# Optimization experiments

Measured on AMD Instinct MI355X. Metric: run time of the kernel, lower is better.

Reference implementation:

```python
import jax, jax.numpy as jnp
import numpy as np

C_CLIP = 10.0  # Bello et al. logit clipping constant (init arg C)


def setup_inputs() -> dict:
    key = jax.random.key(0)
    k1, k2, k3, k4, k5 = jax.random.split(key, 5)
    B, S, D = 64, 2048, 512
    scale = 1.0 / np.sqrt(D)  # ~torch Linear default init scale
    src = jax.random.normal(k1, (B, S, D), dtype=jnp.float32)
    tgt = jax.random.normal(k2, (B, 1, D), dtype=jnp.float32)
    W_q = jax.random.normal(k3, (D, D), dtype=jnp.float32) * scale
    W_ref = jax.random.normal(k4, (D, D), dtype=jnp.float32) * scale
    v = jax.random.uniform(k5, (D,), dtype=jnp.float32)  # uniform_(0, 1) as in source
    return {"src": src, "tgt": tgt, "W_q": W_q, "W_ref": W_ref, "v": v}


def reference(src, tgt, W_q, W_ref, v):
    # h = tanh(W_q(tgt) + W_ref(src))  -> [B, S, D] (tgt broadcasts over S)
    h = jnp.tanh(tgt @ W_q.T + src @ W_ref.T)
    # u = bmm(v, h^T) -> [B, 1, S]
    u = jnp.einsum("bsd,d->bs", h, v)[:, None, :]
    # logit clipping: C * tanh(u)
    logit = C_CLIP * jnp.tanh(u)
    probs = jax.nn.softmax(logit, axis=-1)  # [B, 1, S]
    # d_prime = bmm(probs, src) -> [B, 1, D]  ('Sup' path glimpse)
    d_prime = jnp.einsum("bqs,bsd->bqd", probs, src)
    return (d_prime, probs, logit)
```

## Files before the change

kernel.cpp:

```cpp
#include <hip/hip_runtime.h>
#include <math.h>

#define NB 64
#define NS 2048
#define ND 512
#define MTOT (NB * NS)
#define CCLIP 10.0f

typedef _Float16 f16x8 __attribute__((ext_vector_type(8)));
typedef _Float16 f16x4 __attribute__((ext_vector_type(4)));
typedef float f32x4 __attribute__((ext_vector_type(4)));

__device__ __forceinline__ void gl2lds16(const void* g, void* l) {
  __builtin_amdgcn_global_load_lds(
      (const __attribute__((address_space(1))) void*)(uintptr_t)g,
      (__attribute__((address_space(3))) void*)(uintptr_t)l, 16, 0, 0);
}

__device__ __forceinline__ float tanh_fast(float x) {
  float e = __expf(2.f * x);
  return 1.f - 2.f * __builtin_amdgcn_rcpf(e + 1.f);
}

__global__ __launch_bounds__(256) void cvtw_kernel(
    const float4* __restrict__ w4, _Float16* __restrict__ WhA) {
  const int idx = blockIdx.x * 256 + threadIdx.x;
  const int d = idx >> 7;
  const int k = (idx & 127) << 2;
  float4 x = w4[idx];
  f16x4 o;
  o[0] = (_Float16)x.x; o[1] = (_Float16)x.y;
  o[2] = (_Float16)x.z; o[3] = (_Float16)x.w;
  const int kt = k >> 5;
  const int kg = (k >> 3) & 3;
  const int h = k & 7;
  *(f16x4*)(WhA + ((size_t)((kt * 4 + kg) * 512 + d) * 8 + h)) = o;
}

__global__ __launch_bounds__(256) void qk_kernel(const float* __restrict__ tgt,
                                                 const float* __restrict__ Wq,
                                                 float* __restrict__ q_ws) {
  const int b = blockIdx.x >> 1;
  const int d = ((blockIdx.x & 1) << 8) + threadIdx.x;
  __shared__ float tl[ND];
  tl[threadIdx.x] = tgt[b * ND + threadIdx.x];
  tl[threadIdx.x + 256] = tgt[b * ND + threadIdx.x + 256];
  __syncthreads();
  const float4* wr = (const float4*)(Wq + (size_t)d * ND);
  float acc = 0.f;
#pragma unroll 8
  for (int k4 = 0; k4 < ND / 4; ++k4) {
    float4 w4 = wr[k4];
    acc += w4.x * tl[4 * k4 + 0] + w4.y * tl[4 * k4 + 1] +
           w4.z * tl[4 * k4 + 2] + w4.w * tl[4 * k4 + 3];
  }
  q_ws[b * ND + d] = acc;
}

__global__ __launch_bounds__(256, 2) void gemm_kernel(
    const float* __restrict__ src, const _Float16* __restrict__ WhA,
    const float* __restrict__ q_ws, const float* __restrict__ v,
    float* __restrict__ out_logit, float* __restrict__ out_probs_w) {
  __shared__ __align__(16) _Float16 sA[4 * 64 * 8];
  __shared__ __align__(16) _Float16 sB[4 * 512 * 8];
  __shared__ float ured[4 * 64];

  const int tid = threadIdx.x;
  const int lane = tid & 63;
  const int w = tid >> 6;
  const int s0 = blockIdx.x << 6;
  const int bb = blockIdx.x >> 5;

  const int quad = lane >> 4;
  const int l15 = lane & 15;

  const int ar = tid & 63;
  const int akg = tid >> 6;
  const float4* ap =
      (const float4*)(src + ((size_t)(s0 + ar) << 9)) + akg * 2;
  _Float16* aw = sA + (akg * 64 + ar) * 8;

  const char* gB = (const char*)WhA;

  f32x4 acc[4][8];
#pragma unroll
  for (int i = 0; i < 4; ++i)
#pragma unroll
    for (int j = 0; j < 8; ++j) acc[i][j] = (f32x4){0.f, 0.f, 0.f, 0.f};

  for (int kt = 0; kt < 16; ++kt) {
    __syncthreads();
#pragma unroll
    for (int i = 0; i < 8; ++i) {
      const int c = w * 8 + i;
      gl2lds16(gB + (size_t)kt * 32768 + c * 1024 + lane * 16,
               (char*)sB + c * 1024);
    }
    float4 x0 = ap[kt * 8];
    float4 x1 = ap[kt * 8 + 1];
    f16x8 h;
    h[0] = (_Float16)x0.x; h[1] = (_Float16)x0.y;
    h[2] = (_Float16)x0.z; h[3] = (_Float16)x0.w;
    h[4] = (_Float16)x1.x; h[5] = (_Float16)x1.y;
    h[6] = (_Float16)x1.z; h[7] = (_Float16)x1.w;
    *(f16x8*)aw = h;
    __syncthreads();

    f16x8 af[4], bf[8];
#pragma unroll
    for (int i = 0; i < 4; ++i)
      af[i] = *(const f16x8*)(sA + (quad * 64 + 16 * i + l15) * 8);
#pragma unroll
    for (int j = 0; j < 8; ++j)
      bf[j] = *(const f16x8*)(sB + (quad * 512 + w * 128 + 16 * j + l15) * 8);
#pragma unroll
    for (int i = 0; i < 4; ++i)
#pragma unroll
      for (int j = 0; j < 8; ++j)
        acc[i][j] = __builtin_amdgcn_mfma_f32_16x16x32_f16(af[i], bf[j],
                                                           acc[i][j], 0, 0, 0);
  }

  float pu[4][4];
#pragma unroll
  for (int i = 0; i < 4; ++i)
#pragma unroll
    for (int r = 0; r < 4; ++r) pu[i][r] = 0.f;

#pragma unroll
  for (int j = 0; j < 8; ++j) {
    const int dl = w * 128 + 16 * j + l15;
    const float qq = q_ws[bb * ND + dl];
    const float vv = v[dl];
#pragma unroll
    for (int i = 0; i < 4; ++i) {
      f32x4 a = acc[i][j];
#pragma unroll
      for (int r = 0; r < 4; ++r) pu[i][r] += tanh_fast(a[r] + qq) * vv;
    }
  }

#pragma unroll
  for (int i = 0; i < 4; ++i)
#pragma unroll
    for (int r = 0; r < 4; ++r) {
      float x = pu[i][r];
      x += __shfl_xor(x, 1, 16);
      x += __shfl_xor(x, 2, 16);
      x += __shfl_xor(x, 4, 16);
      x += __shfl_xor(x, 8, 16);
      pu[i][r] = x;
    }

  if (l15 == 0) {
#pragma unroll
    for (int i = 0; i < 4; ++i)
#pragma unroll
      for (int r = 0; r < 4; ++r)
        ured[w * 64 + 16 * i + quad * 4 + r] = pu[i][r];
  }
  __syncthreads();
  if (tid < 64) {
    const float u =
        ured[tid] + ured[64 + tid] + ured[128 + tid] + ured[192 + tid];
    const float lg = CCLIP * tanhf(u);
    out_logit[s0 + tid] = lg;
    out_probs_w[s0 + tid] = expf(lg - CCLIP);
  }
}

__global__ __launch_bounds__(256) void dp_kernel(const float* __restrict__ src,
                                                 const float* __restrict__ w_ws,
                                                 float* __restrict__ dp_ws) {
  const int blk = blockIdx.x;
  const int b = blk >> 4;
  const int ch = (blk >> 1) & 7;
  const int half = blk & 1;
  const int tid = threadIdx.x;
  const int row0 = b * NS + ch * 256;
  const float* base = src + ((size_t)row0 << 9) + (half << 8) + tid;
  float a = 0.f;
#pragma unroll 8
  for (int s = 0; s < 256; ++s) a += w_ws[row0 + s] * base[(size_t)s << 9];
  dp_ws[(size_t)blk * 256 + tid] = a;
}

__global__ __launch_bounds__(256) void fin_kernel(
    const float* __restrict__ dp_ws, float* __restrict__ out_dp,
    float* __restrict__ out_probs) {
  const int b = blockIdx.x;
  const int tid = threadIdx.x;
  __shared__ float red[4];
  __shared__ float s_inv;

  float x = 0.f;
  for (int idx = tid; idx < NS; idx += 256) x += out_probs[b * NS + idx];
#pragma unroll
  for (int m = 32; m; m >>= 1) x += __shfl_xor(x, m, 64);
  if ((tid & 63) == 0) red[tid >> 6] = x;
  __syncthreads();
  if (tid == 0) s_inv = 1.f / (red[0] + red[1] + red[2] + red[3]);
  __syncthreads();
  const float inv = s_inv;

  for (int idx = tid; idx < NS; idx += 256)
    out_probs[b * NS + idx] *= inv;

  for (int d = tid; d < ND; d += 256) {
    const int half = d >> 8;
    const int dl = d & 255;
    float acc = 0.f;
#pragma unroll
    for (int ch = 0; ch < 8; ++ch)
      acc += dp_ws[(size_t)(((b * 8 + ch) << 1) + half) * 256 + dl];
    out_dp[b * ND + d] = acc * inv;
  }
}

extern "C" void kernel_launch(void* const* d_in, const int* in_sizes, int n_in,
                              void* d_out, int out_size, void* d_ws,
                              size_t ws_size, hipStream_t stream) {
  const float* src = (const float*)d_in[0];
  const float* tgt = (const float*)d_in[1];
  const float* Wq = (const float*)d_in[2];
  const float* Wref = (const float*)d_in[3];
  const float* v = (const float*)d_in[4];

  float* out = (float*)d_out;
  float* out_dp = out;
  float* out_probs = out + NB * ND;
  float* out_logit = out + NB * ND + NB * NS;

  char* ws = (char*)d_ws;
  _Float16* WhA = (_Float16*)ws;
  float* q_ws = (float*)(ws + 524288);
  float* dp_ws = (float*)(ws + 655360);

  cvtw_kernel<<<256, 256, 0, stream>>>((const float4*)Wref, WhA);
  qk_kernel<<<2 * NB, 256, 0, stream>>>(tgt, Wq, q_ws);
  gemm_kernel<<<MTOT / 64, 256, 0, stream>>>(src, WhA, q_ws, v, out_logit,
                                             out_probs);
  dp_kernel<<<NB * 16, 256, 0, stream>>>(src, out_probs, dp_ws);
  fin_kernel<<<NB, 256, 0, stream>>>(dp_ws, out_dp, out_probs);
}
```

Baseline: 482.0 us.

## Fuse weighted src reduction into GEMM and double-buffer LDS tiles

The separate dp_kernel is removed. Each GEMM block now computes its own exp-weighted sum of its 64 src rows right after the logits, while those rows are likely still in cache, and writes per-block partials that fin_kernel reduces over 32 chunks. The GEMM main loop double-buffers the A and B LDS tiles, prefetching the next k-tile while MFMAs run, so there is one barrier per iteration instead of two. The A-load thread mapping is also changed so each row is read contiguously. The cost is double the LDS footprint, which may reduce occupancy, and a larger dp workspace.

```diff
diff --git a/kernel.cpp b/kernel.cpp
--- a/kernel.cpp
+++ b/kernel.cpp
@@ -60,10 +60,12 @@
 __global__ __launch_bounds__(256, 2) void gemm_kernel(
     const float* __restrict__ src, const _Float16* __restrict__ WhA,
     const float* __restrict__ q_ws, const float* __restrict__ v,
-    float* __restrict__ out_logit, float* __restrict__ out_probs_w) {
-  __shared__ __align__(16) _Float16 sA[4 * 64 * 8];
-  __shared__ __align__(16) _Float16 sB[4 * 512 * 8];
+    float* __restrict__ out_logit, float* __restrict__ out_probs_w,
+    float* __restrict__ dp_ws) {
+  __shared__ __align__(16) _Float16 sA[2][4 * 64 * 8];
+  __shared__ __align__(16) _Float16 sB[2][4 * 512 * 8];
   __shared__ float ured[4 * 64];
+  __shared__ float wsh[64];
 
   const int tid = threadIdx.x;
   const int lane = tid & 63;
@@ -74,11 +76,11 @@
   const int quad = lane >> 4;
   const int l15 = lane & 15;
 
-  const int ar = tid & 63;
-  const int akg = tid >> 6;
+  const int ar = tid >> 2;
+  const int akg = tid & 3;
   const float4* ap =
       (const float4*)(src + ((size_t)(s0 + ar) << 9)) + akg * 2;
-  _Float16* aw = sA + (akg * 64 + ar) * 8;
+  const int aoff = (akg * 64 + ar) * 8;
 
   const char* gB = (const char*)WhA;
 
@@ -88,37 +90,61 @@
 #pragma unroll
     for (int j = 0; j < 8; ++j) acc[i][j] = (f32x4){0.f, 0.f, 0.f, 0.f};
 
-  for (int kt = 0; kt < 16; ++kt) {
-    __syncthreads();
-#pragma unroll
-    for (int i = 0; i < 8; ++i) {
-      const int c = w * 8 + i;
-      gl2lds16(gB + (size_t)kt * 32768 + c * 1024 + lane * 16,
-               (char*)sB + c * 1024);
-    }
-    float4 x0 = ap[kt * 8];
-    float4 x1 = ap[kt * 8 + 1];
+#pragma unroll
+  for (int i = 0; i < 8; ++i) {
+    const int c = w * 8 + i;
+    gl2lds16(gB + c * 1024 + lane * 16, (char*)&sB[0][0] + c * 1024);
+  }
+  {
+    float4 x0 = ap[0];
+    float4 x1 = ap[1];
     f16x8 h;
     h[0] = (_Float16)x0.x; h[1] = (_Float16)x0.y;
     h[2] = (_Float16)x0.z; h[3] = (_Float16)x0.w;
     h[4] = (_Float16)x1.x; h[5] = (_Float16)x1.y;
     h[6] = (_Float16)x1.z; h[7] = (_Float16)x1.w;
-    *(f16x8*)aw = h;
-    __syncthreads();
-
+    *(f16x8*)(&sA[0][0] + aoff) = h;
+  }
+  __syncthreads();
+
+  int buf = 0;
+  for (int kt = 0; kt < 16; ++kt) {
+    const int nb = buf ^ 1;
+    float4 x0, x1;
+    if (kt < 15) {
+#pragma unroll
+      for (int i = 0; i < 8; ++i) {
+        const int c = w * 8 + i;
+        gl2lds16(gB + (size_t)(kt + 1) * 32768 + c * 1024 + lane * 16,
+                 (char*)&sB[nb][0] + c * 1024);
+      }
+      x0 = ap[(kt + 1) * 8];
+      x1 = ap[(kt + 1) * 8 + 1];
+    }
     f16x8 af[4], bf[8];
 #pragma unroll
     for (int i = 0; i < 4; ++i)
-      af[i] = *(const f16x8*)(sA + (quad * 64 + 16 * i + l15) * 8);
+      af[i] = *(const f16x8*)(&sA[buf][0] + (quad * 64 + 16 * i + l15) * 8);
 #pragma unroll
     for (int j = 0; j < 8; ++j)
-      bf[j] = *(const f16x8*)(sB + (quad * 512 + w * 128 + 16 * j + l15) * 8);
+      bf[j] = *(const f16x8*)(&sB[buf][0] +
+                              (quad * 512 + w * 128 + 16 * j + l15) * 8);
 #pragma unroll
     for (int i = 0; i < 4; ++i)
 #pragma unroll
       for (int j = 0; j < 8; ++j)
         acc[i][j] = __builtin_amdgcn_mfma_f32_16x16x32_f16(af[i], bf[j],
                                                            acc[i][j], 0, 0, 0);
+    if (kt < 15) {
+      f16x8 h;
+      h[0] = (_Float16)x0.x; h[1] = (_Float16)x0.y;
+      h[2] = (_Float16)x0.z; h[3] = (_Float16)x0.w;
+      h[4] = (_Float16)x1.x; h[5] = (_Float16)x1.y;
+      h[6] = (_Float16)x1.z; h[7] = (_Float16)x1.w;
+      *(f16x8*)(&sA[nb][0] + aoff) = h;
+    }
+    __syncthreads();
+    buf = nb;
   }
 
   float pu[4][4];
@@ -165,24 +191,34 @@
         ured[tid] + ured[64 + tid] + ured[128 + tid] + ured[192 + tid];
     const float lg = CCLIP * tanhf(u);
     out_logit[s0 + tid] = lg;
-    out_probs_w[s0 + tid] = expf(lg - CCLIP);
-  }
-}
-
-__global__ __launch_bounds__(256) void dp_kernel(const float* __restrict__ src,
-                                                 const float* __restrict__ w_ws,
-                                                 float* __restrict__ dp_ws) {
-  const int blk = blockIdx.x;
-  const int b = blk >> 4;
-  const int ch = (blk >> 1) & 7;
-  const int half = blk & 1;
-  const int tid = threadIdx.x;
-  const int row0 = b * NS + ch * 256;
-  const float* base = src + ((size_t)row0 << 9) + (half << 8) + tid;
-  float a = 0.f;
-#pragma unroll 8
-  for (int s = 0; s < 256; ++s) a += w_ws[row0 + s] * base[(size_t)s << 9];
-  dp_ws[(size_t)blk * 256 + tid] = a;
+    const float wexp = expf(lg - CCLIP);
+    out_probs_w[s0 + tid] = wexp;
+    wsh[tid] = wexp;
+  }
+  __syncthreads();
+
+  const int c4 = tid & 127;
+  const int half = tid >> 7;
+  const float4* sp = (const float4*)(src + ((size_t)s0 << 9)) + c4;
+  float dx = 0.f, dy = 0.f, dz = 0.f, dw = 0.f;
+  const int r0 = half << 5;
+#pragma unroll 4
+  for (int r = r0; r < r0 + 32; ++r) {
+    const float wr = wsh[r];
+    const float4 x = sp[(size_t)r * 128];
+    dx += wr * x.x; dy += wr * x.y; dz += wr * x.z; dw += wr * x.w;
+  }
+  float4* red4 = (float4*)&sA[0][0];
+  if (half) {
+    float4 o; o.x = dx; o.y = dy; o.z = dz; o.w = dw;
+    red4[c4] = o;
+  }
+  __syncthreads();
+  if (!half) {
+    float4 o = red4[c4];
+    o.x += dx; o.y += dy; o.z += dz; o.w += dw;
+    *(float4*)(dp_ws + (size_t)blockIdx.x * ND + (c4 << 2)) = o;
+  }
 }
 
 __global__ __launch_bounds__(256) void fin_kernel(
@@ -207,12 +243,10 @@
     out_probs[b * NS + idx] *= inv;
 
   for (int d = tid; d < ND; d += 256) {
-    const int half = d >> 8;
-    const int dl = d & 255;
     float acc = 0.f;
-#pragma unroll
-    for (int ch = 0; ch < 8; ++ch)
-      acc += dp_ws[(size_t)(((b * 8 + ch) << 1) + half) * 256 + dl];
+#pragma unroll 8
+    for (int ch = 0; ch < 32; ++ch)
+      acc += dp_ws[(size_t)(b * 32 + ch) * ND + d];
     out_dp[b * ND + d] = acc * inv;
   }
 }
@@ -239,7 +273,6 @@
   cvtw_kernel<<<256, 256, 0, stream>>>((const float4*)Wref, WhA);
   qk_kernel<<<2 * NB, 256, 0, stream>>>(tgt, Wq, q_ws);
   gemm_kernel<<<MTOT / 64, 256, 0, stream>>>(src, WhA, q_ws, v, out_logit,
-                                             out_probs);
-  dp_kernel<<<NB * 16, 256, 0, stream>>>(src, out_probs, dp_ws);
+                                             out_probs, dp_ws);
   fin_kernel<<<NB, 256, 0, stream>>>(dp_ws, out_dp, out_probs);
 }
```

Measured after the change: 447.9 us. -7.1%, faster.
